# Performance work log

Measured on AMD Instinct MI355X. Metric: run time of the kernel, lower is better.

Reference implementation:

```python
import jax, jax.numpy as jnp
import numpy as np

N_EMBED = 1024
NUM_HEADS = 16
HEAD_SIZE = 64  # NUM_HEADS * HEAD_SIZE == N_EMBED
BLOCK_SIZE = 2048


def setup_inputs() -> dict:
    key = jax.random.key(0)
    ks = jax.random.split(key, 9)
    s = 1.0 / np.sqrt(N_EMBED)
    batch_x = jax.random.normal(ks[0], (4, BLOCK_SIZE, N_EMBED), dtype=jnp.float32)
    # stacked per-head linear params: weight [H, E, d], bias [H, d]
    Wq = jax.random.uniform(ks[1], (NUM_HEADS, N_EMBED, HEAD_SIZE), jnp.float32, -s, s)
    Wk = jax.random.uniform(ks[2], (NUM_HEADS, N_EMBED, HEAD_SIZE), jnp.float32, -s, s)
    Wv = jax.random.uniform(ks[3], (NUM_HEADS, N_EMBED, HEAD_SIZE), jnp.float32, -s, s)
    bq = jax.random.uniform(ks[4], (NUM_HEADS, HEAD_SIZE), jnp.float32, -s, s)
    bk = jax.random.uniform(ks[5], (NUM_HEADS, HEAD_SIZE), jnp.float32, -s, s)
    bv = jax.random.uniform(ks[6], (NUM_HEADS, HEAD_SIZE), jnp.float32, -s, s)
    Wp = jax.random.uniform(ks[7], (N_EMBED, N_EMBED), jnp.float32, -s, s)
    bp = jax.random.uniform(ks[8], (N_EMBED,), jnp.float32, -s, s)
    return {"batch_x": batch_x, "Wq": Wq, "Wk": Wk, "Wv": Wv,
            "bq": bq, "bk": bk, "bv": bv, "Wp": Wp, "bp": bp}


def reference(batch_x, Wq, Wk, Wv, bq, bk, bv, Wp, bp):
    B, T, E = batch_x.shape
    # per-head projections: [B, H, T, d]
    q = jnp.einsum('bte,hed->bhtd', batch_x, Wq) + bq[None, :, None, :]
    k = jnp.einsum('bte,hed->bhtd', batch_x, Wk) + bk[None, :, None, :]
    v = jnp.einsum('bte,hed->bhtd', batch_x, Wv) + bv[None, :, None, :]
    scale = 1.0 / jnp.sqrt(jnp.asarray(HEAD_SIZE, batch_x.dtype))
    wei = jnp.einsum('bhtd,bhsd->bhts', q, k) * scale  # [B,H,T,T]
    causal = jnp.tril(jnp.ones((T, T), dtype=bool))
    wei = jnp.where(causal, wei, jnp.asarray(-jnp.inf, wei.dtype))
    wei = jax.nn.softmax(wei, axis=-1)
    out = jnp.einsum('bhts,bhsd->bhtd', wei, v)  # [B,H,T,d]
    # concat heads (head order matches torch.cat over ModuleList)
    out = out.transpose(0, 2, 1, 3).reshape(B, T, NUM_HEADS * HEAD_SIZE)
    return out @ Wp + bp
```

## Files before the change

kernel.cpp:

```cpp
#include <hip/hip_runtime.h>
#include <math.h>

#define B_ 4
#define T_ 2048
#define E_ 1024
#define H_ 16
#define D_ 64

typedef __bf16 bf16_t;
typedef bf16_t bf16x8 __attribute__((ext_vector_type(8)));
typedef float  f32x4  __attribute__((ext_vector_type(4)));
typedef float  f32x16 __attribute__((ext_vector_type(16)));
typedef unsigned short u16x4 __attribute__((ext_vector_type(4)));

static __device__ __forceinline__ unsigned short f2bf(float f) {
    bf16_t h = (bf16_t)f;
    return __builtin_bit_cast(unsigned short, h);
}

#define GLD(gp, lp) __builtin_amdgcn_global_load_lds( \
    (const __attribute__((address_space(1))) unsigned int*)(gp), \
    (__attribute__((address_space(3))) unsigned int*)(lp), 16, 0, 0)

#define BAR() __builtin_amdgcn_s_barrier()
#define WAIT_LGKM0() asm volatile("s_waitcnt lgkmcnt(0)" ::: "memory")

__global__ void cast_x_kernel(const float* __restrict__ in, unsigned short* __restrict__ out, int n4) {
    int i = blockIdx.x * blockDim.x + threadIdx.x;
    if (i >= n4) return;
    float4 v = ((const float4*)in)[i];
    ushort4 o;
    o.x = f2bf(v.x); o.y = f2bf(v.y); o.z = f2bf(v.z); o.w = f2bf(v.w);
    ((ushort4*)out)[i] = o;
}

__global__ void tcast_all(const float* __restrict__ Wq, const float* __restrict__ Wk,
                          const float* __restrict__ Wv, const float* __restrict__ Wp,
                          unsigned short* __restrict__ wf, unsigned short* __restrict__ wpt) {
    __shared__ unsigned short Ts[64 * 66];
    const int grp = blockIdx.y >> 4, yy = blockIdx.y & 15;
    const float* in; unsigned short* out; int yA, S;
    if (grp == 3) { in = Wp; out = wpt; yA = 64;    S = 1024; }
    else {
        in = (grp == 0) ? Wq : (grp == 1) ? Wk : Wv;
        out = wf + (size_t)grp * 1024 * 1024; yA = 65536; S = 64;
    }
    const int tid = threadIdx.x;
    const int r = tid >> 2, c4 = tid & 3;
    const float* ip = in + (size_t)yA * yy + (size_t)(blockIdx.x * 64 + r) * S + c4 * 16;
    #pragma unroll
    for (int j = 0; j < 4; ++j) {
        float4 v = *(const float4*)&ip[j * 4];
        Ts[(c4 * 16 + j * 4 + 0) * 66 + r] = f2bf(v.x);
        Ts[(c4 * 16 + j * 4 + 1) * 66 + r] = f2bf(v.y);
        Ts[(c4 * 16 + j * 4 + 2) * 66 + r] = f2bf(v.z);
        Ts[(c4 * 16 + j * 4 + 3) * 66 + r] = f2bf(v.w);
    }
    __syncthreads();
    unsigned short* op = out + (size_t)(yy * 64 + r) * 1024 + blockIdx.x * 64 + c4 * 16;
    #pragma unroll
    for (int j = 0; j < 4; ++j) {
        u16x4 pk;
        #pragma unroll
        for (int m = 0; m < 4; ++m) pk[m] = Ts[r * 66 + c4 * 16 + j * 4 + m];
        *(u16x4*)&op[j * 4] = pk;
    }
}

__global__ __launch_bounds__(512, 2) void qkv_gemm(
    const unsigned short* __restrict__ xb,
    const unsigned short* __restrict__ wf,
    const float* __restrict__ bq, const float* __restrict__ bk, const float* __restrict__ bv,
    unsigned short* __restrict__ qo, unsigned short* __restrict__ ko,
    unsigned short* __restrict__ vt)
{
    __shared__ __align__(16) unsigned short sm[65536];

    const int tid = threadIdx.x;
    const int w = tid >> 6, lane = tid & 63;
    const int wr = w >> 2, wc = w & 3;
    const int l15 = lane & 15, quad = lane >> 4, lsw = l15 & 7;
    const int m0 = blockIdx.x * 256;
    const int n0 = blockIdx.y * 256;

    f32x4 acc[8][4];
    #pragma unroll
    for (int i = 0; i < 8; ++i)
        #pragma unroll
        for (int j = 0; j < 4; ++j) acc[i][j] = (f32x4){0.f, 0.f, 0.f, 0.f};

    const int swzE = (((lane & 7) ^ (lane >> 3)) * 8);
    const unsigned short* Agb = xb + (size_t)(m0 + w * 16 + (lane >> 3)) * 1024 + swzE;
    const unsigned short* Bgb = wf + (size_t)(n0 + w * 16 + (lane >> 3)) * 1024 + swzE;

    auto stage_half = [&](int t, int which) {
        unsigned short* dst = sm + (t & 1) * 32768 + which * 8192 + w * 1024;
        const unsigned short* src = ((which < 2) ? Agb : Bgb)
                                  + (size_t)((which & 1) * 128) * 1024 + t * 64;
        GLD(src, dst);
        GLD(src + (size_t)8 * 1024, dst + 512);
    };
    auto rdA = [&](int t, int fm, int ks) {
        const int row = wr * 128 + fm * 16 + l15;
        return *(const bf16x8*)&sm[(t & 1) * 32768 + (row >> 7) * 8192
                                   + (row & 127) * 64 + (((ks * 4 + quad) ^ lsw) * 8)];
    };
    auto rdB = [&](int t, int fn, int ks) {
        const int row = wc * 64 + fn * 16 + l15;
        return *(const bf16x8*)&sm[(t & 1) * 32768 + 16384 + (row >> 7) * 8192
                                   + (row & 127) * 64 + (((ks * 4 + quad) ^ lsw) * 8)];
    };

    stage_half(0, 0); stage_half(0, 1); stage_half(0, 2); stage_half(0, 3);
    stage_half(1, 2); stage_half(1, 3);
    asm volatile("s_waitcnt vmcnt(4)" ::: "memory");
    BAR();

    #define MFMA_Q(mb, nb) \
        __builtin_amdgcn_s_setprio(1); \
        _Pragma("unroll") \
        for (int i_ = 0; i_ < 4; ++i_) \
            _Pragma("unroll") \
            for (int j_ = 0; j_ < 2; ++j_) \
                _Pragma("unroll") \
                for (int ks_ = 0; ks_ < 2; ++ks_) \
                    acc[(mb) + i_][(nb) + j_] = __builtin_amdgcn_mfma_f32_16x16x32_bf16( \
                        fA[i_][ks_], fB[(nb) + j_][ks_], acc[(mb) + i_][(nb) + j_], 0, 0, 0); \
        __builtin_amdgcn_s_setprio(0);

    #pragma unroll 1
    for (int it = 0; it < 8; ++it) {
        const int t0 = 2 * it, t1 = 2 * it + 1;
        const bool more = it < 7;
        bf16x8 fA[4][2], fB[4][2];

        #pragma unroll
        for (int m = 0; m < 4; ++m) { fA[m][0] = rdA(t0, m, 0); fA[m][1] = rdA(t0, m, 1); }
        #pragma unroll
        for (int n = 0; n < 2; ++n) { fB[n][0] = rdB(t0, n, 0); fB[n][1] = rdB(t0, n, 1); }
        stage_half(t1, 0);
        BAR(); WAIT_LGKM0();
        MFMA_Q(0, 0);
        BAR();

        #pragma unroll
        for (int n = 0; n < 2; ++n) { fB[2 + n][0] = rdB(t0, 2 + n, 0); fB[2 + n][1] = rdB(t0, 2 + n, 1); }
        stage_half(t1, 1);
        BAR(); WAIT_LGKM0();
        MFMA_Q(0, 2);
        BAR();

        #pragma unroll
        for (int m = 0; m < 4; ++m) { fA[m][0] = rdA(t0, 4 + m, 0); fA[m][1] = rdA(t0, 4 + m, 1); }
        if (more) stage_half(t0 + 2, 2);
        BAR(); WAIT_LGKM0();
        MFMA_Q(4, 2);
        BAR();

        if (more) {
            stage_half(t0 + 2, 3);
            asm volatile("s_waitcnt vmcnt(4)" ::: "memory");
        } else {
            asm volatile("s_waitcnt vmcnt(0)" ::: "memory");
        }
        BAR();
        MFMA_Q(4, 0);
        BAR();

        #pragma unroll
        for (int m = 0; m < 4; ++m) { fA[m][0] = rdA(t1, m, 0); fA[m][1] = rdA(t1, m, 1); }
        #pragma unroll
        for (int n = 0; n < 2; ++n) { fB[n][0] = rdB(t1, n, 0); fB[n][1] = rdB(t1, n, 1); }
        if (more) stage_half(t0 + 2, 0);
        BAR(); WAIT_LGKM0();
        MFMA_Q(0, 0);
        BAR();

        #pragma unroll
        for (int n = 0; n < 2; ++n) { fB[2 + n][0] = rdB(t1, 2 + n, 0); fB[2 + n][1] = rdB(t1, 2 + n, 1); }
        if (more) stage_half(t0 + 2, 1);
        BAR(); WAIT_LGKM0();
        MFMA_Q(0, 2);
        BAR();

        #pragma unroll
        for (int m = 0; m < 4; ++m) { fA[m][0] = rdA(t1, 4 + m, 0); fA[m][1] = rdA(t1, 4 + m, 1); }
        if (more) stage_half(t1 + 2, 2);
        BAR(); WAIT_LGKM0();
        MFMA_Q(4, 2);
        BAR();

        if (more) {
            stage_half(t1 + 2, 3);
            asm volatile("s_waitcnt vmcnt(4)" ::: "memory");
        } else {
            asm volatile("s_waitcnt vmcnt(0)" ::: "memory");
        }
        BAR();
        MFMA_Q(4, 0);
        BAR();
    }
    #undef MFMA_Q

    const int which = n0 >> 10;
    const int nb = n0 & 1023;
    if (which < 2) {
        const float* bias = which ? bk : bq;
        unsigned short* outp = which ? ko : qo;
        const float sc = which ? 1.f : 0.125f;
        #pragma unroll
        for (int fm = 0; fm < 8; ++fm)
            #pragma unroll
            for (int fn = 0; fn < 4; ++fn) {
                int colg = nb + wc * 64 + fn * 16 + l15;
                int h = colg >> 6, d = colg & 63;
                float bi = bias[colg];
                #pragma unroll
                for (int r = 0; r < 4; ++r) {
                    int row = m0 + wr * 128 + fm * 16 + quad * 4 + r;
                    int b = row >> 11, t = row & 2047;
                    outp[(((size_t)b * 16 + h) * 2048 + t) * 64 + d] = f2bf((acc[fm][fn][r] + bi) * sc);
                }
            }
    } else {
        const int b = m0 >> 11;
        for (int mh = 0; mh < 2; ++mh)
            for (int nh = 0; nh < 2; ++nh) {
                __syncthreads();
                if (wr == mh && (wc >> 1) == nh) {
                    const int cc = wc & 1;
                    #pragma unroll
                    for (int fm = 0; fm < 8; ++fm)
                        #pragma unroll
                        for (int fn = 0; fn < 4; ++fn) {
                            int colL = cc * 64 + fn * 16 + l15;
                            int colg = nb + nh * 128 + colL;
                            float bi = bv[colg];
                            u16x4 pk;
                            #pragma unroll
                            for (int r = 0; r < 4; ++r) pk[r] = f2bf(acc[fm][fn][r] + bi);
                            *(u16x4*)&sm[colL * 136 + fm * 16 + quad * 4] = pk;
                        }
                }
                __syncthreads();
                const int nl = tid >> 2, tq = tid & 3;
                const int colg = nb + nh * 128 + nl;
                const int h = colg >> 6, d = colg & 63;
                const int t0 = (m0 & 2047) + mh * 128;
                unsigned short* dst = vt + (((size_t)b * 16 + h) * 64 + d) * 2048 + t0 + tq * 32;
                #pragma unroll
                for (int j = 0; j < 4; ++j)
                    *(float4*)&dst[j * 8] = *(const float4*)&sm[nl * 136 + tq * 32 + j * 8];
            }
    }
}

__global__ __launch_bounds__(256, 3) void attn_kernel(
    const unsigned short* __restrict__ q, const unsigned short* __restrict__ k,
    const unsigned short* __restrict__ vt, unsigned short* __restrict__ att2)
{
    __shared__ __align__(16) unsigned short Ks[64 * 64];
    __shared__ __align__(16) unsigned short Vs[64 * 64];
    __shared__ __align__(16) unsigned short Ps[4][32 * 64];

    const int tid = threadIdx.x;
    const int w = tid >> 6, lane = tid & 63;
    const int l31 = lane & 31, h = lane >> 5;
    const int bh = blockIdx.x;
    const int sw_q = l31 & 7;

    unsigned short* Pw = Ps[w];
    const unsigned short* kb = k  + (size_t)bh * 2048 * 64;
    const unsigned short* vb = vt + (size_t)bh * 64 * 2048;
    const int sr = tid >> 2;
    const int sc0 = tid & 3;
    const int ssw = sr & 7;

    for (int leg = 0; leg < 2; ++leg) {
        const int qtile = leg ? (15 - (int)blockIdx.y) : (int)blockIdx.y;
        const int qb0 = qtile * 128;
        const int qg = qb0 + w * 32 + l31;
        const int qmin = qb0 + w * 32, qmax = qmin + 31;
        const int trips = 2 * qtile + 2;

        bf16x8 fQ[4];
        {
            const unsigned short* qp = q + ((size_t)bh * 2048 + qg) * 64 + h * 8;
            #pragma unroll
            for (int ks = 0; ks < 4; ++ks) fQ[ks] = *(const bf16x8*)&qp[ks * 16];
        }

        f32x16 O[2];
        #pragma unroll
        for (int nt = 0; nt < 2; ++nt)
            #pragma unroll
            for (int i = 0; i < 16; ++i) O[nt][i] = 0.f;
        float lsum = 0.f;

        for (int jt = 0; jt < trips; ++jt) {
            __syncthreads();
            {
                const unsigned short* kg = kb + (size_t)(jt * 64) * 64;
                const unsigned short* vg = vb + jt * 64;
                #pragma unroll
                for (int it = 0; it < 2; ++it) {
                    int ci = sc0 + 4 * it;
                    int sw = ((ci ^ ssw)) * 8;
                    *(float4*)&Ks[sr * 64 + sw] = *(const float4*)&kg[(size_t)sr * 64 + ci * 8];
                    *(float4*)&Vs[sr * 64 + sw] = *(const float4*)&vg[(size_t)sr * 2048 + ci * 8];
                }
            }
            __syncthreads();

            const int key0 = jt * 64;
            if (key0 <= qmax) {
                f32x16 S[2];
                #pragma unroll
                for (int kt = 0; kt < 2; ++kt)
                    #pragma unroll
                    for (int i = 0; i < 16; ++i) S[kt][i] = 0.f;
                __builtin_amdgcn_s_setprio(1);
                #pragma unroll
                for (int kt = 0; kt < 2; ++kt) {
                    const int row = kt * 32 + l31, rs = row & 7;
                    #pragma unroll
                    for (int ks = 0; ks < 4; ++ks) {
                        bf16x8 aK = *(const bf16x8*)&Ks[row * 64 + ((2 * ks + h) ^ rs) * 8];
                        S[kt] = __builtin_amdgcn_mfma_f32_32x32x16_bf16(aK, fQ[ks], S[kt], 0, 0, 0);
                    }
                }
                __builtin_amdgcn_s_setprio(0);

                const bool need_mask = (key0 + 63) > qmin;
                #pragma unroll
                for (int kt = 0; kt < 2; ++kt) {
                    #pragma unroll
                    for (int g = 0; g < 4; ++g) {
                        u16x4 pk;
                        #pragma unroll
                        for (int r = 0; r < 4; ++r) {
                            float p = __expf(S[kt][4 * g + r]);
                            if (need_mask) {
                                int key = key0 + kt * 32 + 8 * g + 4 * h + r;
                                if (key > qg) p = 0.f;
                            }
                            lsum += p;
                            pk[r] = f2bf(p);
                        }
                        *(u16x4*)&Pw[l31 * 64 + ((4 * kt + g) ^ sw_q) * 8 + 4 * h] = pk;
                    }
                }
                __builtin_amdgcn_s_setprio(1);
                #pragma unroll
                for (int ks2 = 0; ks2 < 4; ++ks2) {
                    bf16x8 aP = *(const bf16x8*)&Pw[l31 * 64 + ((2 * ks2 + h) ^ sw_q) * 8];
                    #pragma unroll
                    for (int nt = 0; nt < 2; ++nt) {
                        const int drow = nt * 32 + l31;
                        bf16x8 bV = *(const bf16x8*)&Vs[drow * 64 + ((2 * ks2 + h) ^ (drow & 7)) * 8];
                        O[nt] = __builtin_amdgcn_mfma_f32_32x32x16_bf16(aP, bV, O[nt], 0, 0, 0);
                    }
                }
                __builtin_amdgcn_s_setprio(0);
            }
        }

        lsum += __shfl_xor(lsum, 32);
        const float inv = 1.f / lsum;

        unsigned short* ob = att2 + ((size_t)bh * 2048 + qb0 + w * 32) * 64;
        #pragma unroll
        for (int g = 0; g < 4; ++g)
            #pragma unroll
            for (int r = 0; r < 4; ++r) {
                const int qy = 8 * g + 4 * h + r;
                const float iv = __shfl(inv, qy);
                #pragma unroll
                for (int nt = 0; nt < 2; ++nt)
                    ob[(size_t)qy * 64 + nt * 32 + l31] = f2bf(O[nt][4 * g + r] * iv);
            }
    }
}

__global__ __launch_bounds__(256) void proj_gemm(
    const unsigned short* __restrict__ A,
    const unsigned short* __restrict__ wpt,
    const float* __restrict__ bp,
    float* __restrict__ out)
{
    __shared__ __align__(16) unsigned short sm[16384];
    unsigned short* As = sm;
    unsigned short* Bs = sm + 8192;

    const int tid = threadIdx.x;
    const int w = tid >> 6, lane = tid & 63, l15 = lane & 15, quad = lane >> 4;
    const int m0 = blockIdx.x * 128;
    const int n0 = blockIdx.y * 128;

    f32x4 acc[2][8];
    #pragma unroll
    for (int s = 0; s < 2; ++s)
        #pragma unroll
        for (int n = 0; n < 8; ++n) acc[s][n] = (f32x4){0.f, 0.f, 0.f, 0.f};

    const unsigned short* Ag = A + (size_t)(m0 >> 11) * 16 * 131072
                                 + (size_t)((m0 & 2047) + 32 * w + (lane >> 3)) * 64 + (lane & 7) * 8;
    const unsigned short* Bg = wpt + (size_t)(n0 + 32 * w + (lane >> 3)) * 1024 + (lane & 7) * 8;
    unsigned short* Al = As + (32 * w) * 64;
    unsigned short* Bl = Bs + (32 * w) * 64;

    for (int k0 = 0; k0 < 1024; k0 += 64) {
        __syncthreads();
        const size_t aoff = (size_t)(k0 >> 6) * 131072;
        #pragma unroll
        for (int j = 0; j < 4; ++j) {
            GLD(Ag + aoff + (size_t)(8 * j) * 64, Al + (8 * j) * 64);
            GLD(Bg + (size_t)(8 * j) * 1024 + k0, Bl + (8 * j) * 64);
        }
        __syncthreads();
        #pragma unroll
        for (int ks = 0; ks < 2; ++ks) {
            bf16x8 a0 = *(const bf16x8*)&As[(32 * w + l15) * 64 + ks * 32 + quad * 8];
            bf16x8 a1 = *(const bf16x8*)&As[(32 * w + 16 + l15) * 64 + ks * 32 + quad * 8];
            #pragma unroll
            for (int n = 0; n < 8; ++n) {
                bf16x8 b = *(const bf16x8*)&Bs[(16 * n + l15) * 64 + ks * 32 + quad * 8];
                acc[0][n] = __builtin_amdgcn_mfma_f32_16x16x32_bf16(a0, b, acc[0][n], 0, 0, 0);
                acc[1][n] = __builtin_amdgcn_mfma_f32_16x16x32_bf16(a1, b, acc[1][n], 0, 0, 0);
            }
        }
    }

    #pragma unroll
    for (int s = 0; s < 2; ++s)
        #pragma unroll
        for (int n = 0; n < 8; ++n) {
            float bi = bp[n0 + 16 * n + l15];
            #pragma unroll
            for (int r = 0; r < 4; ++r) {
                int row = m0 + 32 * w + 16 * s + quad * 4 + r;
                out[(size_t)row * 1024 + n0 + 16 * n + l15] = acc[s][n][r] + bi;
            }
        }
}

extern "C" void kernel_launch(void* const* d_in, const int* in_sizes, int n_in,
                              void* d_out, int out_size, void* d_ws, size_t ws_size,
                              hipStream_t stream) {
    const float* x  = (const float*)d_in[0];
    const float* Wq = (const float*)d_in[1];
    const float* Wk = (const float*)d_in[2];
    const float* Wv = (const float*)d_in[3];
    const float* bq = (const float*)d_in[4];
    const float* bk = (const float*)d_in[5];
    const float* bv = (const float*)d_in[6];
    const float* Wp = (const float*)d_in[7];
    const float* bp = (const float*)d_in[8];
    float* out = (float*)d_out;

    const size_t nx = (size_t)B_ * T_ * E_;
    unsigned short* base = (unsigned short*)d_ws;
    unsigned short* xb  = base;
    unsigned short* qb  = xb + nx;
    unsigned short* kb  = qb + nx;
    unsigned short* vtb = kb + nx;
    unsigned short* atb = vtb + nx;
    unsigned short* wf  = atb + nx;
    unsigned short* wpt = wf + 3072 * 1024;

    cast_x_kernel<<<(int)(nx / 4 + 255) / 256, 256, 0, stream>>>(x, xb, (int)(nx / 4));
    tcast_all<<<dim3(16, 64), 256, 0, stream>>>(Wq, Wk, Wv, Wp, wf, wpt);
    qkv_gemm<<<dim3(32, 12), 512, 0, stream>>>(xb, wf, bq, bk, bv, qb, kb, vtb);
    attn_kernel<<<dim3(64, 8), 256, 0, stream>>>(qb, kb, vtb, atb);
    proj_gemm<<<dim3(64, 8), 256, 0, stream>>>(atb, wpt, bp, out);
}
```

Before: 273.0 us.

## Split attention key tiles across wave pairs and pass P via lane shuffles

The attention kernel now gives each block a 64-row query tile instead of 128, and launches twice as many blocks. Each pair of waves shares 32 query rows, with each wave handling half of every 64-key tile. Partial outputs and row sums are reduced through the reused K/V shared buffers at the end. The probability tile is no longer staged through a per-wave LDS buffer; it is rearranged into the MFMA A-operand layout with cross-half shuffles. The LDS saving allows launch bounds of 4 blocks per CU. The cost is one extra reduction pass and barriers, plus the K/V tile being loaded once per 64 query rows instead of once per 128.

```diff
diff --git a/kernel.cpp b/kernel.cpp
--- a/kernel.cpp
+++ b/kernel.cpp
@@ -12,10 +12,14 @@
 typedef float  f32x4  __attribute__((ext_vector_type(4)));
 typedef float  f32x16 __attribute__((ext_vector_type(16)));
 typedef unsigned short u16x4 __attribute__((ext_vector_type(4)));
+typedef unsigned int   u32x4 __attribute__((ext_vector_type(4)));
 
 static __device__ __forceinline__ unsigned short f2bf(float f) {
     bf16_t h = (bf16_t)f;
     return __builtin_bit_cast(unsigned short, h);
+}
+static __device__ __forceinline__ unsigned int pk2(float a, float b) {
+    return (unsigned int)f2bf(a) | ((unsigned int)f2bf(b) << 16);
 }
 
 #define GLD(gp, lp) __builtin_amdgcn_global_load_lds( \
@@ -255,21 +259,20 @@
     }
 }
 
-__global__ __launch_bounds__(256, 3) void attn_kernel(
+__global__ __launch_bounds__(256, 4) void attn_kernel(
     const unsigned short* __restrict__ q, const unsigned short* __restrict__ k,
     const unsigned short* __restrict__ vt, unsigned short* __restrict__ att2)
 {
     __shared__ __align__(16) unsigned short Ks[64 * 64];
     __shared__ __align__(16) unsigned short Vs[64 * 64];
-    __shared__ __align__(16) unsigned short Ps[4][32 * 64];
+    __shared__ float Ls[2][64];
 
     const int tid = threadIdx.x;
     const int w = tid >> 6, lane = tid & 63;
     const int l31 = lane & 31, h = lane >> 5;
+    const int qhalf = w >> 1, ksel = w & 1;
     const int bh = blockIdx.x;
-    const int sw_q = l31 & 7;
-
-    unsigned short* Pw = Ps[w];
+
     const unsigned short* kb = k  + (size_t)bh * 2048 * 64;
     const unsigned short* vb = vt + (size_t)bh * 64 * 2048;
     const int sr = tid >> 2;
@@ -277,11 +280,11 @@
     const int ssw = sr & 7;
 
     for (int leg = 0; leg < 2; ++leg) {
-        const int qtile = leg ? (15 - (int)blockIdx.y) : (int)blockIdx.y;
-        const int qb0 = qtile * 128;
-        const int qg = qb0 + w * 32 + l31;
-        const int qmin = qb0 + w * 32, qmax = qmin + 31;
-        const int trips = 2 * qtile + 2;
+        const int qt = leg ? (31 - (int)blockIdx.y) : (int)blockIdx.y;
+        const int qb0 = qt * 64;
+        const int qmin = qb0 + qhalf * 32;
+        const int qg = qmin + l31;
+        const int trips = qt + 1;
 
         bf16x8 fQ[4];
         {
@@ -312,53 +315,68 @@
             }
             __syncthreads();
 
-            const int key0 = jt * 64;
-            if (key0 <= qmax) {
-                f32x16 S[2];
-                #pragma unroll
-                for (int kt = 0; kt < 2; ++kt)
-                    #pragma unroll
-                    for (int i = 0; i < 16; ++i) S[kt][i] = 0.f;
+            const int wk0 = jt * 64 + ksel * 32;
+            if (wk0 <= qmin + 31) {
+                f32x16 S;
+                #pragma unroll
+                for (int i = 0; i < 16; ++i) S[i] = 0.f;
                 __builtin_amdgcn_s_setprio(1);
-                #pragma unroll
-                for (int kt = 0; kt < 2; ++kt) {
-                    const int row = kt * 32 + l31, rs = row & 7;
+                {
+                    const int row = ksel * 32 + l31, rs = l31 & 7;
                     #pragma unroll
                     for (int ks = 0; ks < 4; ++ks) {
                         bf16x8 aK = *(const bf16x8*)&Ks[row * 64 + ((2 * ks + h) ^ rs) * 8];
-                        S[kt] = __builtin_amdgcn_mfma_f32_32x32x16_bf16(aK, fQ[ks], S[kt], 0, 0, 0);
+                        S = __builtin_amdgcn_mfma_f32_32x32x16_bf16(aK, fQ[ks], S, 0, 0, 0);
                     }
                 }
                 __builtin_amdgcn_s_setprio(0);
 
-                const bool need_mask = (key0 + 63) > qmin;
-                #pragma unroll
-                for (int kt = 0; kt < 2; ++kt) {
+                const bool need_mask = (wk0 + 31) > qmin;
+                unsigned int e0[4], e1[4];
+                #pragma unroll
+                for (int g = 0; g < 4; ++g) {
+                    float p[4];
                     #pragma unroll
-                    for (int g = 0; g < 4; ++g) {
-                        u16x4 pk;
-                        #pragma unroll
-                        for (int r = 0; r < 4; ++r) {
-                            float p = __expf(S[kt][4 * g + r]);
-                            if (need_mask) {
-                                int key = key0 + kt * 32 + 8 * g + 4 * h + r;
-                                if (key > qg) p = 0.f;
-                            }
-                            lsum += p;
-                            pk[r] = f2bf(p);
+                    for (int r = 0; r < 4; ++r) {
+                        float pv = __expf(S[4 * g + r]);
+                        if (need_mask) {
+                            int key = wk0 + 8 * g + 4 * h + r;
+                            if (key > qg) pv = 0.f;
                         }
-                        *(u16x4*)&Pw[l31 * 64 + ((4 * kt + g) ^ sw_q) * 8 + 4 * h] = pk;
+                        p[r] = pv;
+                        lsum += pv;
                     }
-                }
+                    e0[g] = pk2(p[0], p[1]);
+                    e1[g] = pk2(p[2], p[3]);
+                }
+
+                bf16x8 aP[2];
+                #pragma unroll
+                for (int s = 0; s < 2; ++s) {
+                    const int ge = 2 * s, go = 2 * s + 1;
+                    unsigned int own0 = h ? e0[go] : e0[ge];
+                    unsigned int snd0 = h ? e0[ge] : e0[go];
+                    unsigned int rcv0 = (unsigned int)__shfl_xor((int)snd0, 32);
+                    unsigned int own1 = h ? e1[go] : e1[ge];
+                    unsigned int snd1 = h ? e1[ge] : e1[go];
+                    unsigned int rcv1 = (unsigned int)__shfl_xor((int)snd1, 32);
+                    u32x4 t;
+                    t[0] = h ? rcv0 : own0;
+                    t[1] = h ? rcv1 : own1;
+                    t[2] = h ? own0 : rcv0;
+                    t[3] = h ? own1 : rcv1;
+                    aP[s] = __builtin_bit_cast(bf16x8, t);
+                }
+
                 __builtin_amdgcn_s_setprio(1);
                 #pragma unroll
-                for (int ks2 = 0; ks2 < 4; ++ks2) {
-                    bf16x8 aP = *(const bf16x8*)&Pw[l31 * 64 + ((2 * ks2 + h) ^ sw_q) * 8];
+                for (int s = 0; s < 2; ++s) {
+                    const int ks2 = 2 * ksel + s;
                     #pragma unroll
                     for (int nt = 0; nt < 2; ++nt) {
                         const int drow = nt * 32 + l31;
                         bf16x8 bV = *(const bf16x8*)&Vs[drow * 64 + ((2 * ks2 + h) ^ (drow & 7)) * 8];
-                        O[nt] = __builtin_amdgcn_mfma_f32_32x32x16_bf16(aP, bV, O[nt], 0, 0, 0);
+                        O[nt] = __builtin_amdgcn_mfma_f32_32x32x16_bf16(aP[s], bV, O[nt], 0, 0, 0);
                     }
                 }
                 __builtin_amdgcn_s_setprio(0);
@@ -366,19 +384,38 @@
         }
 
         lsum += __shfl_xor(lsum, 32);
-        const float inv = 1.f / lsum;
-
-        unsigned short* ob = att2 + ((size_t)bh * 2048 + qb0 + w * 32) * 64;
-        #pragma unroll
-        for (int g = 0; g < 4; ++g)
-            #pragma unroll
-            for (int r = 0; r < 4; ++r) {
-                const int qy = 8 * g + 4 * h + r;
-                const float iv = __shfl(inv, qy);
-                #pragma unroll
-                for (int nt = 0; nt < 2; ++nt)
-                    ob[(size_t)qy * 64 + nt * 32 + l31] = f2bf(O[nt][4 * g + r] * iv);
-            }
+
+        __syncthreads();
+        float* ObH = (float*)(qhalf ? (void*)Vs : (void*)Ks);
+        if (ksel) {
+            #pragma unroll
+            for (int nt = 0; nt < 2; ++nt)
+                #pragma unroll
+                for (int i = 0; i < 16; ++i)
+                    ObH[(nt * 16 + i) * 64 + lane] = O[nt][i];
+            if (lane < 32) Ls[qhalf][l31] = lsum;
+        }
+        __syncthreads();
+        if (!ksel) {
+            #pragma unroll
+            for (int nt = 0; nt < 2; ++nt)
+                #pragma unroll
+                for (int i = 0; i < 16; ++i)
+                    O[nt][i] += ObH[(nt * 16 + i) * 64 + lane];
+            const float inv = 1.f / (lsum + Ls[qhalf][l31]);
+
+            unsigned short* ob = att2 + ((size_t)bh * 2048 + qmin) * 64;
+            #pragma unroll
+            for (int g = 0; g < 4; ++g)
+                #pragma unroll
+                for (int r = 0; r < 4; ++r) {
+                    const int qy = 8 * g + 4 * h + r;
+                    const float iv = __shfl(inv, qy);
+                    #pragma unroll
+                    for (int nt = 0; nt < 2; ++nt)
+                        ob[(size_t)qy * 64 + nt * 32 + l31] = f2bf(O[nt][4 * g + r] * iv);
+                }
+        }
     }
 }
 
@@ -471,6 +508,6 @@
     cast_x_kernel<<<(int)(nx / 4 + 255) / 256, 256, 0, stream>>>(x, xb, (int)(nx / 4));
     tcast_all<<<dim3(16, 64), 256, 0, stream>>>(Wq, Wk, Wv, Wp, wf, wpt);
     qkv_gemm<<<dim3(32, 12), 512, 0, stream>>>(xb, wf, bq, bk, bv, qb, kb, vtb);
-    attn_kernel<<<dim3(64, 8), 256, 0, stream>>>(qb, kb, vtb, atb);
+    attn_kernel<<<dim3(64, 16), 256, 0, stream>>>(qb, kb, vtb, atb);
     proj_gemm<<<dim3(64, 8), 256, 0, stream>>>(atb, wpt, bp, out);
 }
```

New measurement: 277.8 us. About the same (+1.8%).

## Double-buffer K/V via async global-to-LDS loads and keep P in registers

Applied to the files above, without the earlier changes.

The attention kernel now double-buffers K and V tiles in shared memory, using global_load_lds direct copies so the next tile is prefetched while the current one is computed. This replaces the two per-iteration barriers with a single wait and barrier. The probability tile is no longer written to and read back from LDS; it is packed into registers and exchanged between half-waves with cross-lane shuffles to form the MFMA A operand. Occupancy is raised to 4 blocks per CU, which the freed LDS allows, at the cost of tighter register limits and extra shuffle instructions.

```diff
diff --git a/kernel.cpp b/kernel.cpp
--- a/kernel.cpp
+++ b/kernel.cpp
@@ -12,10 +12,14 @@
 typedef float  f32x4  __attribute__((ext_vector_type(4)));
 typedef float  f32x16 __attribute__((ext_vector_type(16)));
 typedef unsigned short u16x4 __attribute__((ext_vector_type(4)));
+typedef unsigned int   u32x4 __attribute__((ext_vector_type(4)));
 
 static __device__ __forceinline__ unsigned short f2bf(float f) {
     bf16_t h = (bf16_t)f;
     return __builtin_bit_cast(unsigned short, h);
+}
+static __device__ __forceinline__ unsigned int pk2(float a, float b) {
+    return (unsigned int)f2bf(a) | ((unsigned int)f2bf(b) << 16);
 }
 
 #define GLD(gp, lp) __builtin_amdgcn_global_load_lds( \
@@ -255,32 +259,30 @@
     }
 }
 
-__global__ __launch_bounds__(256, 3) void attn_kernel(
+__global__ __launch_bounds__(256, 4) void attn_kernel(
     const unsigned short* __restrict__ q, const unsigned short* __restrict__ k,
     const unsigned short* __restrict__ vt, unsigned short* __restrict__ att2)
 {
-    __shared__ __align__(16) unsigned short Ks[64 * 64];
-    __shared__ __align__(16) unsigned short Vs[64 * 64];
-    __shared__ __align__(16) unsigned short Ps[4][32 * 64];
+    __shared__ __align__(16) unsigned short KV[2][2][4096];
 
     const int tid = threadIdx.x;
     const int w = tid >> 6, lane = tid & 63;
     const int l31 = lane & 31, h = lane >> 5;
     const int bh = blockIdx.x;
-    const int sw_q = l31 & 7;
-
-    unsigned short* Pw = Ps[w];
+    const int rs = l31 & 7;
+
     const unsigned short* kb = k  + (size_t)bh * 2048 * 64;
     const unsigned short* vb = vt + (size_t)bh * 64 * 2048;
-    const int sr = tid >> 2;
-    const int sc0 = tid & 3;
-    const int ssw = sr & 7;
+
+    const int swz = ((lane & 7) ^ (lane >> 3)) * 8;
+    const unsigned short* Kg = kb + (size_t)(16 * w + (lane >> 3)) * 64 + swz;
+    const unsigned short* Vg = vb + (size_t)(16 * w + (lane >> 3)) * 2048 + swz;
 
     for (int leg = 0; leg < 2; ++leg) {
         const int qtile = leg ? (15 - (int)blockIdx.y) : (int)blockIdx.y;
         const int qb0 = qtile * 128;
-        const int qg = qb0 + w * 32 + l31;
         const int qmin = qb0 + w * 32, qmax = qmin + 31;
+        const int qg = qmin + l31;
         const int trips = 2 * qtile + 2;
 
         bf16x8 fQ[4];
@@ -297,20 +299,27 @@
             for (int i = 0; i < 16; ++i) O[nt][i] = 0.f;
         float lsum = 0.f;
 
+        {
+            unsigned short* dK = &KV[0][0][w * 1024];
+            unsigned short* dV = &KV[0][1][w * 1024];
+            GLD(Kg, dK); GLD(Kg + 512, dK + 512);
+            GLD(Vg, dV); GLD(Vg + 8 * 2048, dV + 512);
+        }
+        asm volatile("s_waitcnt vmcnt(0)" ::: "memory");
+        BAR();
+
         for (int jt = 0; jt < trips; ++jt) {
-            __syncthreads();
-            {
-                const unsigned short* kg = kb + (size_t)(jt * 64) * 64;
-                const unsigned short* vg = vb + jt * 64;
-                #pragma unroll
-                for (int it = 0; it < 2; ++it) {
-                    int ci = sc0 + 4 * it;
-                    int sw = ((ci ^ ssw)) * 8;
-                    *(float4*)&Ks[sr * 64 + sw] = *(const float4*)&kg[(size_t)sr * 64 + ci * 8];
-                    *(float4*)&Vs[sr * 64 + sw] = *(const float4*)&vg[(size_t)sr * 2048 + ci * 8];
-                }
-            }
-            __syncthreads();
+            const int buf = jt & 1;
+            if (jt + 1 < trips) {
+                unsigned short* dK = &KV[buf ^ 1][0][w * 1024];
+                unsigned short* dV = &KV[buf ^ 1][1][w * 1024];
+                const unsigned short* sK = Kg + (size_t)(jt + 1) * 4096;
+                const unsigned short* sV = Vg + (jt + 1) * 64;
+                GLD(sK, dK); GLD(sK + 512, dK + 512);
+                GLD(sV, dV); GLD(sV + 8 * 2048, dV + 512);
+            }
+            const unsigned short* Ks = KV[buf][0];
+            const unsigned short* Vs = KV[buf][1];
 
             const int key0 = jt * 64;
             if (key0 <= qmax) {
@@ -322,7 +331,7 @@
                 __builtin_amdgcn_s_setprio(1);
                 #pragma unroll
                 for (int kt = 0; kt < 2; ++kt) {
-                    const int row = kt * 32 + l31, rs = row & 7;
+                    const int row = kt * 32 + l31;
                     #pragma unroll
                     for (int ks = 0; ks < 4; ++ks) {
                         bf16x8 aK = *(const bf16x8*)&Ks[row * 64 + ((2 * ks + h) ^ rs) * 8];
@@ -332,43 +341,61 @@
                 __builtin_amdgcn_s_setprio(0);
 
                 const bool need_mask = (key0 + 63) > qmin;
-                #pragma unroll
-                for (int kt = 0; kt < 2; ++kt) {
+                unsigned int e0[2][4], e1[2][4];
+                #pragma unroll
+                for (int kt = 0; kt < 2; ++kt)
                     #pragma unroll
                     for (int g = 0; g < 4; ++g) {
-                        u16x4 pk;
+                        float p[4];
                         #pragma unroll
                         for (int r = 0; r < 4; ++r) {
-                            float p = __expf(S[kt][4 * g + r]);
+                            float pv = __expf(S[kt][4 * g + r]);
                             if (need_mask) {
                                 int key = key0 + kt * 32 + 8 * g + 4 * h + r;
-                                if (key > qg) p = 0.f;
+                                if (key > qg) pv = 0.f;
                             }
-                            lsum += p;
-                            pk[r] = f2bf(p);
+                            p[r] = pv;
+                            lsum += pv;
                         }
-                        *(u16x4*)&Pw[l31 * 64 + ((4 * kt + g) ^ sw_q) * 8 + 4 * h] = pk;
+                        e0[kt][g] = pk2(p[0], p[1]);
+                        e1[kt][g] = pk2(p[2], p[3]);
                     }
-                }
+
                 __builtin_amdgcn_s_setprio(1);
                 #pragma unroll
                 for (int ks2 = 0; ks2 < 4; ++ks2) {
-                    bf16x8 aP = *(const bf16x8*)&Pw[l31 * 64 + ((2 * ks2 + h) ^ sw_q) * 8];
+                    const int kt = ks2 >> 1, s = ks2 & 1;
+                    const int ge = 2 * s, go = 2 * s + 1;
+                    unsigned int own0 = h ? e0[kt][go] : e0[kt][ge];
+                    unsigned int snd0 = h ? e0[kt][ge] : e0[kt][go];
+                    unsigned int rcv0 = (unsigned int)__shfl_xor((int)snd0, 32);
+                    unsigned int own1 = h ? e1[kt][go] : e1[kt][ge];
+                    unsigned int snd1 = h ? e1[kt][ge] : e1[kt][go];
+                    unsigned int rcv1 = (unsigned int)__shfl_xor((int)snd1, 32);
+                    u32x4 t;
+                    t[0] = h ? rcv0 : own0;
+                    t[1] = h ? rcv1 : own1;
+                    t[2] = h ? own0 : rcv0;
+                    t[3] = h ? own1 : rcv1;
+                    bf16x8 aP = __builtin_bit_cast(bf16x8, t);
                     #pragma unroll
                     for (int nt = 0; nt < 2; ++nt) {
                         const int drow = nt * 32 + l31;
-                        bf16x8 bV = *(const bf16x8*)&Vs[drow * 64 + ((2 * ks2 + h) ^ (drow & 7)) * 8];
+                        bf16x8 bV = *(const bf16x8*)&Vs[drow * 64 + ((2 * ks2 + h) ^ rs) * 8];
                         O[nt] = __builtin_amdgcn_mfma_f32_32x32x16_bf16(aP, bV, O[nt], 0, 0, 0);
                     }
                 }
                 __builtin_amdgcn_s_setprio(0);
             }
+
+            asm volatile("s_waitcnt vmcnt(0)" ::: "memory");
+            BAR();
         }
 
         lsum += __shfl_xor(lsum, 32);
         const float inv = 1.f / lsum;
 
-        unsigned short* ob = att2 + ((size_t)bh * 2048 + qb0 + w * 32) * 64;
+        unsigned short* ob = att2 + ((size_t)bh * 2048 + qmin) * 64;
         #pragma unroll
         for (int g = 0; g < 4; ++g)
             #pragma unroll
```

After: 276.8 us. About the same (+1.4%).
